# Performance work log

Measured on AMD Instinct MI355X. Metric: run time of the kernel, lower is better.

The kernel has to match this reference:

```python
import jax, jax.numpy as jnp
import numpy as np

B, T, W, CIN, H, COUT = 256, 512, 64, 2, 256, 2
FIN = W * CIN  # 128


def setup_inputs() -> dict:
    key = jax.random.key(0)
    ks = jax.random.split(key, 9)
    s = lambda *sh: 1.0 / np.sqrt(sh[0])
    x = jax.random.normal(ks[0], (B, T, W, CIN), dtype=jnp.float32)
    W1 = jax.random.normal(ks[1], (FIN, H), dtype=jnp.float32) * s(FIN)
    b1 = jnp.zeros((H,), dtype=jnp.float32)
    Wk = jax.random.normal(ks[2], (H, 3 * H), dtype=jnp.float32) * s(H)
    Wr = jax.random.normal(ks[3], (H, 3 * H), dtype=jnp.float32) * s(H)
    bi = jnp.zeros((3 * H,), dtype=jnp.float32)
    br = jnp.zeros((3 * H,), dtype=jnp.float32)
    W2 = jax.random.normal(ks[4], (2 * H, W * COUT), dtype=jnp.float32) * s(2 * H)
    b2 = jnp.zeros((W * COUT,), dtype=jnp.float32)
    return {"x": x, "W1": W1, "b1": b1, "Wk": Wk, "Wr": Wr, "bi": bi, "br": br, "W2": W2, "b2": b2}


def _gru_relu(xg, Wr, br):
    # xg: (T, B, 3H) precomputed input-side gates (x @ Wk + bi)
    # Keras GRU v2: reset_after=True, recurrent_activation=sigmoid, activation=relu
    Hd = Wr.shape[0]
    h0 = jnp.zeros((xg.shape[1], Hd), dtype=xg.dtype)

    def step(h, xg_t):
        rec = h @ Wr + br                     # (B, 3H)
        xz, xr, xh = jnp.split(xg_t, 3, axis=-1)
        rz, rr, rh = jnp.split(rec, 3, axis=-1)
        z = jax.nn.sigmoid(xz + rz)
        r = jax.nn.sigmoid(xr + rr)
        hh = jax.nn.relu(xh + r * rh)
        h_new = z * h + (1.0 - z) * hh
        return h_new, None

    h_last, _ = jax.lax.scan(step, h0, xg)
    return h_last


def reference(x, W1, b1, Wk, Wr, bi, br, W2, b2):
    b = x.shape[0]
    xf = x.reshape(b, T, FIN)                 # Reshape((T, W*CIN))
    h1 = jax.nn.relu(xf @ W1 + b1)            # Dense(hidden, relu): (B, T, H)
    xg = jnp.transpose(h1 @ Wk + bi, (1, 0, 2))  # (T, B, 3H)
    h_last = _gru_relu(xg, Wr, br)            # (B, H); output == final_state
    feat = jnp.concatenate([h_last, h_last], axis=-1)  # (B, 2H)
    y = feat @ W2 + b2                        # (B, W*COUT)
    return y.reshape(b, W, COUT)
```

## Files before the change

### kernel.cpp

```cpp
#include <hip/hip_runtime.h>

typedef unsigned short u16;
typedef unsigned int u32;
typedef float f32x4 __attribute__((ext_vector_type(4)));
typedef __bf16 bf16x8 __attribute__((ext_vector_type(8)));

#define TB 256
#define TT 512

__device__ __forceinline__ u16 f2b(float f) {
  u32 x = __float_as_uint(f);
  return (u16)((x + 0x7fffu + ((x >> 16) & 1u)) >> 16);
}
__device__ __forceinline__ u32 pkbf(float a, float b) {
  u32 r;
  asm("v_cvt_pk_bf16_f32 %0, %1, %2" : "=v"(r) : "v"(a), "v"(b));
  return r;
}
__device__ __forceinline__ float blo(u32 u) { return __uint_as_float(u << 16); }
__device__ __forceinline__ float bhi(u32 u) { return __uint_as_float(u & 0xffff0000u); }
__device__ __forceinline__ float sigm(float x) {
  return __builtin_amdgcn_rcpf(1.f + __expf(-x));
}

__global__ void tcast_kernel(const float* __restrict__ in, u16* __restrict__ out, int K, int N) {
  int idx = blockIdx.x * blockDim.x + threadIdx.x;
  if (idx < K * N) {
    int k = idx / N, n = idx % N;
    out[n * K + k] = f2b(in[idx]);
  }
}

__global__ void wrperm_kernel(const float* __restrict__ in, u16* __restrict__ out) {
  int idx = blockIdx.x * blockDim.x + threadIdx.x;
  if (idx < 256 * 768) {
    int k = idx / 768, n = idx % 768;
    int gate = n >> 8, c = n & 255;
    int w = c >> 5, cc = c & 31, l15 = cc >> 1, grp = cc & 1;
    int nt = gate * 2 + grp;
    out[((((w * 6 + nt) << 4) + l15) << 8) + k] = f2b(in[idx]);
  }
}

__global__ void biasmod_kernel(const float* __restrict__ bi, const float* __restrict__ br,
                               float* __restrict__ bm) {
  int n = blockIdx.x * blockDim.x + threadIdx.x;
  if (n < 768) bm[n] = bi[n] + (n < 512 ? br[n] : 0.f);
}

template<int KT, int MODE, int CASTA, int TCv>
__device__ void gemm_tile(char* smem_c, const void* __restrict__ Av, const u16* __restrict__ Bt,
                          const float* __restrict__ bias, u16* __restrict__ C, int t0,
                          int bm, int bn) {
  constexpr int K = KT * 32;
  const u16* A = (const u16*)Av;
  const float* Af = (const float*)Av;
  u16* As = (u16*)smem_c;
  u16* Bs = (u16*)(smem_c + 10240);
  const int tid = threadIdx.x;
  const bool act = (tid < 256);
  const int lane = tid & 63, wid = tid >> 6;
  const int l15 = lane & 15, l4 = lane >> 4;
  const int qm = ((wid & 3) >> 1) * 64, qn = (wid & 1) * 64;

  const int c0 = tid & 255, c1 = (tid & 255) + 256;
  const int r0 = c0 >> 2, r1 = c1 >> 2;
  int ar0, ar1;
  if (MODE == 0) {
    ar0 = bm * 128 + r0;
    ar1 = bm * 128 + r1;
  } else if (TCv == 64) {
    ar0 = (2 * bm + (r0 >> 6)) * 512 + t0 + (r0 & 63);
    ar1 = (2 * bm + (r1 >> 6)) * 512 + t0 + (r1 & 63);
  } else {
    ar0 = bm * 512 + t0 + r0;
    ar1 = bm * 512 + t0 + r1;
  }
  const size_t ga0 = (size_t)ar0 * K + (c0 & 3) * 8;
  const size_t ga1 = (size_t)ar1 * K + (c1 & 3) * 8;
  const size_t gb0 = (size_t)(bn * 128 + r0) * K + (c0 & 3) * 8;
  const size_t gb1 = (size_t)(bn * 128 + r1) * K + (c1 & 3) * 8;
  const int sa0 = r0 * 40 + (c0 & 3) * 8;
  const int sa1 = r1 * 40 + (c1 & 3) * 8;

#define LOADA(ga, ko, dst)                                                       \
  if (CASTA) {                                                                   \
    const float* p = Af + (ga) + (ko);                                           \
    const f32x4 v0 = *(const f32x4*)(p);                                         \
    const f32x4 v1 = *(const f32x4*)(p + 4);                                     \
    (dst).x = pkbf(v0[0], v0[1]); (dst).y = pkbf(v0[2], v0[3]);                  \
    (dst).z = pkbf(v1[0], v1[1]); (dst).w = pkbf(v1[2], v1[3]);                  \
  } else {                                                                       \
    (dst) = *(const uint4*)(A + (ga) + (ko));                                    \
  }

  uint4 ra0 = {}, ra1 = {}, rb0 = {}, rb1 = {};
  if (act) {
    LOADA(ga0, 0, ra0);
    LOADA(ga1, 0, ra1);
    rb0 = *(const uint4*)(Bt + gb0);
    rb1 = *(const uint4*)(Bt + gb1);
  }
  f32x4 acc[4][4] = {};

  for (int kt = 0; kt < KT; ++kt) {
    __syncthreads();
    if (act) {
      *(uint4*)(As + sa0) = ra0;
      *(uint4*)(As + sa1) = ra1;
      *(uint4*)(Bs + sa0) = rb0;
      *(uint4*)(Bs + sa1) = rb1;
    }
    __syncthreads();
    if (act) {
      if (kt + 1 < KT) {
        const int ko = (kt + 1) * 32;
        LOADA(ga0, ko, ra0);
        LOADA(ga1, ko, ra1);
        rb0 = *(const uint4*)(Bt + gb0 + ko);
        rb1 = *(const uint4*)(Bt + gb1 + ko);
      }
      bf16x8 af[4], bfr[4];
#pragma unroll
      for (int mt = 0; mt < 4; ++mt)
        af[mt] = *(const bf16x8*)(As + (qm + mt * 16 + l15) * 40 + l4 * 8);
#pragma unroll
      for (int nt = 0; nt < 4; ++nt)
        bfr[nt] = *(const bf16x8*)(Bs + (qn + nt * 16 + l15) * 40 + l4 * 8);
#pragma unroll
      for (int mt = 0; mt < 4; ++mt)
#pragma unroll
        for (int nt = 0; nt < 4; ++nt)
          acc[mt][nt] = __builtin_amdgcn_mfma_f32_16x16x32_bf16(af[mt], bfr[nt], acc[mt][nt], 0, 0, 0);
    }
  }
#undef LOADA

  if (act) {
#pragma unroll
    for (int mt = 0; mt < 4; ++mt)
#pragma unroll
      for (int nt = 0; nt < 4; ++nt) {
        const int n = bn * 128 + qn + nt * 16 + l15;
        const float bv = bias[n];
#pragma unroll
        for (int j = 0; j < 4; ++j) {
          const int rloc = qm + mt * 16 + l4 * 4 + j;
          float v = acc[mt][nt][j] + bv;
          if (MODE == 0) {
            v = fmaxf(v, 0.f);
            C[(size_t)(bm * 128 + rloc) * 256 + n] = f2b(v);
          } else {
            C[((size_t)bm * 128 + rloc) * 768 + n] = f2b(v);
          }
        }
      }
  }
}

__global__ __launch_bounds__(256) void gemm1_kernel(const float* __restrict__ x,
                                                    const u16* __restrict__ W1T,
                                                    const float* __restrict__ b1,
                                                    u16* __restrict__ h1) {
  __shared__ alignas(16) char smem_c[20480];
  gemm_tile<4, 0, 1, 64>(smem_c, x, W1T, b1, h1, 0, blockIdx.x, blockIdx.y);
}
template<int TCv>
__global__ __launch_bounds__(256) void gemm2_kernel(const u16* __restrict__ h1,
                                                    const u16* __restrict__ WkT,
                                                    const float* __restrict__ biasM,
                                                    u16* __restrict__ xg, int t0) {
  __shared__ alignas(16) char smem_c[20480];
  gemm_tile<8, 1, 0, TCv>(smem_c, h1, WkT, biasM, xg, t0, blockIdx.x, blockIdx.y);
}

template<int TCv>
__global__ __launch_bounds__(512, 1) void fused_kernel(
    const u16* __restrict__ xrd, u16* __restrict__ xwr,
    const u16* __restrict__ WrP, const float* __restrict__ br,
    float* __restrict__ hstate, const u16* __restrict__ h1A,
    const u16* __restrict__ WkT, const float* __restrict__ biasM,
    int t0, int do_gemm) {
  __shared__ alignas(16) char smem_c[82048];
  const int tid = threadIdx.x;

  if (blockIdx.x < 16) {
    u16* hb0 = (u16*)smem_c;
    u16* hb1 = (u16*)(smem_c + 8448);
    u16* xs0 = (u16*)(smem_c + 16896);
    u16* xs1 = (u16*)(smem_c + 41728);
    const int g = blockIdx.x;
    const int lane = tid & 63, wid = tid >> 6;
    const int l15 = lane & 15, l4 = lane >> 4;

    bf16x8 bw[8][6];
#pragma unroll
    for (int kk = 0; kk < 8; ++kk)
#pragma unroll
      for (int nt = 0; nt < 6; ++nt)
        bw[kk][nt] = *(const bf16x8*)(WrP + ((((wid * 6 + nt) << 4) + l15) << 8) + kk * 32 + l4 * 8);

    const int cbase = wid * 32 + l15 * 2;
    const float brh0 = br[512 + cbase];
    const float brh1 = br[512 + cbase + 1];
    const int rs = tid >> 5, ksl = (tid & 31) * 8;
    const u16* xg_row = xrd + (size_t)(g * 16 + rs) * TCv * 768 + ksl;
    u16* xw0 = xs0 + rs * 776 + ksl;
    u16* xw1 = xs1 + rs * 776 + ksl;

    f32x4 h0v, h1v;
    if (t0 == 0) {
      h0v = {0.f, 0.f, 0.f, 0.f};
      h1v = {0.f, 0.f, 0.f, 0.f};
    } else {
#pragma unroll
      for (int j = 0; j < 4; ++j) {
        float2 ld = *(const float2*)(hstate + ((size_t)g * 16 + l4 * 4 + j) * 256 + cbase);
        h0v[j] = ld.x; h1v[j] = ld.y;
      }
    }
#pragma unroll
    for (int j = 0; j < 4; ++j)
      *(u32*)(hb0 + (l4 * 4 + j) * 264 + cbase) = pkbf(h0v[j], h1v[j]);

    {
      const uint4 s0 = *(const uint4*)(xg_row);
      const uint4 s1 = *(const uint4*)(xg_row + 256);
      const uint4 s2 = *(const uint4*)(xg_row + 512);
      *(uint4*)(xw0) = s0;
      *(uint4*)(xw0 + 256) = s1;
      *(uint4*)(xw0 + 512) = s2;
    }
    __syncthreads();

#define GRU_STEP(SRC, DST, XRD, XWR, TL)                                                    \
  {                                                                                         \
    const int tn = ((TL) + 1 < TCv) ? ((TL) + 1) : (TCv - 1);                               \
    const u16* xq = xg_row + (size_t)tn * 768;                                              \
    const uint4 s0 = *(const uint4*)(xq);                                                   \
    const uint4 s1 = *(const uint4*)(xq + 256);                                             \
    const uint4 s2 = *(const uint4*)(xq + 512);                                             \
    f32x4 a0 = {}, a2 = {}, a4 = {};                                                        \
    _Pragma("unroll")                                                                       \
    for (int kk = 0; kk < 8; ++kk) {                                                        \
      const bf16x8 a = *(const bf16x8*)((SRC) + l15 * 264 + kk * 32 + l4 * 8);              \
      a0 = __builtin_amdgcn_mfma_f32_16x16x32_bf16(a, bw[kk][0], a0, 0, 0, 0);              \
      a2 = __builtin_amdgcn_mfma_f32_16x16x32_bf16(a, bw[kk][2], a2, 0, 0, 0);              \
      a4 = __builtin_amdgcn_mfma_f32_16x16x32_bf16(a, bw[kk][4], a4, 0, 0, 0);              \
    }                                                                                       \
    u32 xz_[4], xr_[4], xh_[4];                                                             \
    _Pragma("unroll")                                                                       \
    for (int j = 0; j < 4; ++j) {                                                           \
      const u16* xr2 = (XRD) + (l4 * 4 + j) * 776 + cbase;                                  \
      xz_[j] = *(const u32*)(xr2);                                                          \
      xr_[j] = *(const u32*)(xr2 + 256);                                                    \
      xh_[j] = *(const u32*)(xr2 + 512);                                                    \
    }                                                                                       \
    f32x4 a1 = {}, a3 = {}, a5 = {};                                                        \
    _Pragma("unroll")                                                                       \
    for (int kk = 0; kk < 8; ++kk) {                                                        \
      const bf16x8 a = *(const bf16x8*)((SRC) + l15 * 264 + kk * 32 + l4 * 8);              \
      a1 = __builtin_amdgcn_mfma_f32_16x16x32_bf16(a, bw[kk][1], a1, 0, 0, 0);              \
      a3 = __builtin_amdgcn_mfma_f32_16x16x32_bf16(a, bw[kk][3], a3, 0, 0, 0);              \
      a5 = __builtin_amdgcn_mfma_f32_16x16x32_bf16(a, bw[kk][5], a5, 0, 0, 0);              \
    }                                                                                       \
    *(uint4*)(XWR) = s0;                                                                    \
    *(uint4*)((XWR) + 256) = s1;                                                            \
    *(uint4*)((XWR) + 512) = s2;                                                            \
    _Pragma("unroll")                                                                       \
    for (int j = 0; j < 4; ++j) {                                                           \
      const float z0 = sigm(blo(xz_[j]) + a0[j]);                                           \
      const float r0 = sigm(blo(xr_[j]) + a2[j]);                                           \
      const float hh0 = fmaxf(fmaf(r0, a4[j] + brh0, blo(xh_[j])), 0.f);                    \
      h0v[j] = fmaf(z0, h0v[j] - hh0, hh0);                                                 \
    }                                                                                       \
    _Pragma("unroll")                                                                       \
    for (int j = 0; j < 4; ++j) {                                                           \
      const float z1 = sigm(bhi(xz_[j]) + a1[j]);                                           \
      const float r1 = sigm(bhi(xr_[j]) + a3[j]);                                           \
      const float hh1 = fmaxf(fmaf(r1, a5[j] + brh1, bhi(xh_[j])), 0.f);                    \
      h1v[j] = fmaf(z1, h1v[j] - hh1, hh1);                                                 \
      *(u32*)((DST) + (l4 * 4 + j) * 264 + cbase) = pkbf(h0v[j], h1v[j]);                   \
    }                                                                                       \
    __syncthreads();                                                                        \
  }

    for (int tl = 0; tl < TCv; tl += 2) {
      GRU_STEP(hb0, hb1, xs0, xw1, tl);
      GRU_STEP(hb1, hb0, xs1, xw0, tl + 1);
    }
#undef GRU_STEP

#pragma unroll
    for (int j = 0; j < 4; ++j) {
      float2 st = {h0v[j], h1v[j]};
      *(float2*)(hstate + ((size_t)g * 16 + l4 * 4 + j) * 256 + cbase) = st;
    }
  } else {
    if (!do_gemm) return;
    constexpr int NT = (TCv == 64) ? 768 : 1536;
    const int t0g = t0 + TCv;
    for (int tix = (int)blockIdx.x - 16; tix < NT; tix += 768) {
      const int bm = (TCv == 64) ? (tix & 127) : (tix & 255);
      const int bn = (TCv == 64) ? (tix >> 7) : (tix >> 8);
      gemm_tile<8, 1, 0, TCv>(smem_c, h1A, WkT, biasM, xwr, t0g, bm, bn);
    }
  }
}

__global__ void out_kernel(const float* __restrict__ h, const float* __restrict__ W2,
                           const float* __restrict__ b2, float* __restrict__ y) {
  const int bb = blockIdx.x, j = threadIdx.x;
  const float* hr = h + (size_t)bb * 256;
  float s = b2[j];
  for (int i = 0; i < 256; ++i)
    s = fmaf(hr[i], W2[i * 128 + j] + W2[(i + 256) * 128 + j], s);
  y[(size_t)bb * 128 + j] = s;
}

extern "C" void kernel_launch(void* const* d_in, const int* in_sizes, int n_in,
                              void* d_out, int out_size, void* d_ws, size_t ws_size,
                              hipStream_t stream) {
  const float* x  = (const float*)d_in[0];
  const float* W1 = (const float*)d_in[1];
  const float* b1 = (const float*)d_in[2];
  const float* Wk = (const float*)d_in[3];
  const float* Wr = (const float*)d_in[4];
  const float* bi = (const float*)d_in[5];
  const float* br = (const float*)d_in[6];
  const float* W2 = (const float*)d_in[7];
  const float* b2 = (const float*)d_in[8];
  float* y = (float*)d_out;

  const size_t NEED128 = 67108864ull + 2 * 50331648ull + 65536ull + 2 * 393216ull +
                         262144ull + 4096ull;
  const size_t NEED64  = 67108864ull + 2 * 25165824ull + 65536ull + 2 * 393216ull +
                         262144ull + 4096ull;
  if (ws_size < NEED64) return;
  const bool big = (ws_size >= NEED128);
  const size_t xgsz = big ? 50331648ull : 25165824ull;

  char* ws = (char*)d_ws;
  u16* h1    = (u16*)ws;  ws += 67108864;
  u16* xg0   = (u16*)ws;  ws += xgsz;
  u16* xg1   = (u16*)ws;  ws += xgsz;
  u16* W1T   = (u16*)ws;  ws += 65536;
  u16* WkT   = (u16*)ws;  ws += 393216;
  u16* WrP   = (u16*)ws;  ws += 393216;
  float* hstate = (float*)ws; ws += 262144;
  float* biasM  = (float*)ws;

  tcast_kernel<<<128, 256, 0, stream>>>(W1, W1T, 128, 256);
  tcast_kernel<<<768, 256, 0, stream>>>(Wk, WkT, 256, 768);
  wrperm_kernel<<<768, 256, 0, stream>>>(Wr, WrP);
  biasmod_kernel<<<3, 256, 0, stream>>>(bi, br, biasM);
  gemm1_kernel<<<dim3(1024, 2), 256, 0, stream>>>(x, W1T, b1, h1);
  if (big) {
    gemm2_kernel<128><<<dim3(256, 6), 256, 0, stream>>>(h1, WkT, biasM, xg0, 0);
    for (int c = 0; c < 4; ++c) {
      const u16* xrd = (c & 1) ? xg1 : xg0;
      u16* xwr = (c & 1) ? xg0 : xg1;
      fused_kernel<128><<<784, 512, 0, stream>>>(xrd, xwr, WrP, br, hstate, h1, WkT, biasM,
                                                 c * 128, (c < 3) ? 1 : 0);
    }
  } else {
    gemm2_kernel<64><<<dim3(128, 6), 256, 0, stream>>>(h1, WkT, biasM, xg0, 0);
    for (int c = 0; c < 8; ++c) {
      const u16* xrd = (c & 1) ? xg1 : xg0;
      u16* xwr = (c & 1) ? xg0 : xg1;
      fused_kernel<64><<<784, 512, 0, stream>>>(xrd, xwr, WrP, br, hstate, h1, WkT, biasM,
                                                c * 64, (c < 7) ? 1 : 0);
    }
  }
  out_kernel<<<256, 128, 0, stream>>>(hstate, W2, b2, y);
}
```

Before: 965.6 us.

## Defer part of the input dense layer into the recurrent kernels and merge prep launches

On the large-workspace path, the standalone first dense layer now computes only the time slices needed for the first input-gate chunk (t < 256). The remaining slices are computed by the otherwise idle GEMM blocks inside the first two fused recurrent launches, so that work overlaps with the sequential GRU steps. Each fused launch produces exactly the h1 rows that the next chunk's input-gate GEMM reads. The three weight-cast/permute kernels and the bias kernel are also merged into one prep launch to cut launch overhead. The cost is heavier GEMM-block work in the fused launches and tighter ordering dependencies across chunks.

```diff
diff --git a/kernel.cpp b/kernel.cpp
--- a/kernel.cpp
+++ b/kernel.cpp
@@ -23,29 +23,28 @@
   return __builtin_amdgcn_rcpf(1.f + __expf(-x));
 }
 
-__global__ void tcast_kernel(const float* __restrict__ in, u16* __restrict__ out, int K, int N) {
-  int idx = blockIdx.x * blockDim.x + threadIdx.x;
-  if (idx < K * N) {
-    int k = idx / N, n = idx % N;
-    out[n * K + k] = f2b(in[idx]);
-  }
-}
-
-__global__ void wrperm_kernel(const float* __restrict__ in, u16* __restrict__ out) {
-  int idx = blockIdx.x * blockDim.x + threadIdx.x;
-  if (idx < 256 * 768) {
-    int k = idx / 768, n = idx % 768;
-    int gate = n >> 8, c = n & 255;
-    int w = c >> 5, cc = c & 31, l15 = cc >> 1, grp = cc & 1;
-    int nt = gate * 2 + grp;
-    out[((((w * 6 + nt) << 4) + l15) << 8) + k] = f2b(in[idx]);
-  }
-}
-
-__global__ void biasmod_kernel(const float* __restrict__ bi, const float* __restrict__ br,
-                               float* __restrict__ bm) {
-  int n = blockIdx.x * blockDim.x + threadIdx.x;
-  if (n < 768) bm[n] = bi[n] + (n < 512 ? br[n] : 0.f);
+__global__ __launch_bounds__(256) void prep_kernel(
+    const float* __restrict__ W1, const float* __restrict__ Wk, const float* __restrict__ Wr,
+    const float* __restrict__ bi, const float* __restrict__ br,
+    u16* __restrict__ W1T, u16* __restrict__ WkT, u16* __restrict__ WrP,
+    float* __restrict__ biasM) {
+  const int gt = blockIdx.x * 256 + threadIdx.x;
+  if (gt < 32768) {
+    const int k = gt >> 8, n = gt & 255;
+    W1T[n * 128 + k] = f2b(W1[gt]);
+  }
+  for (int idx = gt; idx < 196608; idx += 131072) {
+    const int k = idx / 768, n = idx % 768;
+    WkT[(size_t)n * 256 + k] = f2b(Wk[idx]);
+  }
+  for (int idx = gt; idx < 196608; idx += 131072) {
+    const int k = idx / 768, n = idx % 768;
+    const int gate = n >> 8, c = n & 255;
+    const int w = c >> 5, cc = c & 31, l15 = cc >> 1, grp = cc & 1;
+    const int nt = gate * 2 + grp;
+    WrP[((((w * 6 + nt) << 4) + l15) << 8) + k] = f2b(Wr[idx]);
+  }
+  if (gt < 768) biasM[gt] = bi[gt] + (gt < 512 ? br[gt] : 0.f);
 }
 
 template<int KT, int MODE, int CASTA, int TCv>
@@ -165,6 +164,14 @@
   __shared__ alignas(16) char smem_c[20480];
   gemm_tile<4, 0, 1, 64>(smem_c, x, W1T, b1, h1, 0, blockIdx.x, blockIdx.y);
 }
+__global__ __launch_bounds__(256) void gemm1r_kernel(const float* __restrict__ x,
+                                                     const u16* __restrict__ W1T,
+                                                     const float* __restrict__ b1,
+                                                     u16* __restrict__ h1) {
+  __shared__ alignas(16) char smem_c[20480];
+  const int bm = (blockIdx.x & 255) * 4 + (blockIdx.x >> 8);
+  gemm_tile<4, 0, 1, 64>(smem_c, x, W1T, b1, h1, 0, bm, blockIdx.y);
+}
 template<int TCv>
 __global__ __launch_bounds__(256) void gemm2_kernel(const u16* __restrict__ h1,
                                                     const u16* __restrict__ WkT,
@@ -180,7 +187,9 @@
     const u16* __restrict__ WrP, const float* __restrict__ br,
     float* __restrict__ hstate, const u16* __restrict__ h1A,
     const u16* __restrict__ WkT, const float* __restrict__ biasM,
-    int t0, int do_gemm) {
+    const float* __restrict__ x, const u16* __restrict__ W1T,
+    const float* __restrict__ b1, u16* __restrict__ h1w,
+    int t0, int ng2, int g1range) {
   __shared__ alignas(16) char smem_c[82048];
   const int tid = threadIdx.x;
 
@@ -297,13 +306,18 @@
       *(float2*)(hstate + ((size_t)g * 16 + l4 * 4 + j) * 256 + cbase) = st;
     }
   } else {
-    if (!do_gemm) return;
-    constexpr int NT = (TCv == 64) ? 768 : 1536;
     const int t0g = t0 + TCv;
-    for (int tix = (int)blockIdx.x - 16; tix < NT; tix += 768) {
-      const int bm = (TCv == 64) ? (tix & 127) : (tix & 255);
-      const int bn = (TCv == 64) ? (tix >> 7) : (tix >> 8);
-      gemm_tile<8, 1, 0, TCv>(smem_c, h1A, WkT, biasM, xwr, t0g, bm, bn);
+    const int ntot = ng2 + ((g1range >= 0) ? 512 : 0);
+    for (int tix = (int)blockIdx.x - 16; tix < ntot; tix += 768) {
+      if (tix < ng2) {
+        const int bm = (TCv == 64) ? (tix & 127) : (tix & 255);
+        const int bn = (TCv == 64) ? (tix >> 7) : (tix >> 8);
+        gemm_tile<8, 1, 0, TCv>(smem_c, h1A, WkT, biasM, xwr, t0g, bm, bn);
+      } else {
+        const int sub = tix - ng2;
+        const int bmg = (sub >> 1) * 4 + g1range;
+        gemm_tile<4, 0, 1, 64>(smem_c, x, W1T, b1, h1w, 0, bmg, sub & 1);
+      }
     }
   }
 }
@@ -350,26 +364,26 @@
   float* hstate = (float*)ws; ws += 262144;
   float* biasM  = (float*)ws;
 
-  tcast_kernel<<<128, 256, 0, stream>>>(W1, W1T, 128, 256);
-  tcast_kernel<<<768, 256, 0, stream>>>(Wk, WkT, 256, 768);
-  wrperm_kernel<<<768, 256, 0, stream>>>(Wr, WrP);
-  biasmod_kernel<<<3, 256, 0, stream>>>(bi, br, biasM);
-  gemm1_kernel<<<dim3(1024, 2), 256, 0, stream>>>(x, W1T, b1, h1);
+  prep_kernel<<<512, 256, 0, stream>>>(W1, Wk, Wr, bi, br, W1T, WkT, WrP, biasM);
   if (big) {
+    gemm1r_kernel<<<dim3(512, 2), 256, 0, stream>>>(x, W1T, b1, h1);
     gemm2_kernel<128><<<dim3(256, 6), 256, 0, stream>>>(h1, WkT, biasM, xg0, 0);
     for (int c = 0; c < 4; ++c) {
       const u16* xrd = (c & 1) ? xg1 : xg0;
       u16* xwr = (c & 1) ? xg0 : xg1;
-      fused_kernel<128><<<784, 512, 0, stream>>>(xrd, xwr, WrP, br, hstate, h1, WkT, biasM,
-                                                 c * 128, (c < 3) ? 1 : 0);
+      fused_kernel<128><<<784, 512, 0, stream>>>(
+          xrd, xwr, WrP, br, hstate, h1, WkT, biasM, x, W1T, b1, h1,
+          c * 128, (c < 3) ? 1536 : 0, (c < 2) ? (c + 2) : -1);
     }
   } else {
+    gemm1_kernel<<<dim3(1024, 2), 256, 0, stream>>>(x, W1T, b1, h1);
     gemm2_kernel<64><<<dim3(128, 6), 256, 0, stream>>>(h1, WkT, biasM, xg0, 0);
     for (int c = 0; c < 8; ++c) {
       const u16* xrd = (c & 1) ? xg1 : xg0;
       u16* xwr = (c & 1) ? xg0 : xg1;
-      fused_kernel<64><<<784, 512, 0, stream>>>(xrd, xwr, WrP, br, hstate, h1, WkT, biasM,
-                                                c * 64, (c < 7) ? 1 : 0);
+      fused_kernel<64><<<784, 512, 0, stream>>>(
+          xrd, xwr, WrP, br, hstate, h1, WkT, biasM, x, W1T, b1, h1,
+          c * 64, (c < 7) ? 768 : 0, -1);
     }
   }
   out_kernel<<<256, 128, 0, stream>>>(hstate, W2, b2, y);
```

Result: no change. 949.2 us, median of 2 (-1.7%).
